# Kernel optimization log

Hardware: AMD Instinct MI355X
Metric: run time of the kernel (lower is better)

## Reference

```python
import jax, jax.numpy as jnp
import numpy as np

P, D, M, B = 32000, 128, 2, 4096
INIT_STD = 0.01


def setup_inputs() -> dict:
    key = jax.random.key(0)
    k1, k2, k3 = jax.random.split(key, 3)
    x = jax.random.randint(k1, (B, M), 0, P)                       # token indices
    W = INIT_STD * jax.random.normal(k2, (D, P), dtype=jnp.float32)
    V = INIT_STD * jax.random.normal(k3, (P, D), dtype=jnp.float32)
    return {"x": x, "W": W, "V": V}


def reference(x, W, V):
    # Original: one_hot(x, p).sum(1).T -> [p, B]; W @ x_sum == gather columns of W
    # at the token indices and sum over the m positions (identical math, no [B,p]
    # one-hot or dense GEMM materialized).
    hidden = jax.nn.relu(W[:, x].sum(axis=2))   # W[:, x]: [d, B, m] -> [d, B]
    logits = (V @ hidden).T                      # [p, B].T -> [B, p]
    return logits
```

## Files before the change

kernel.cpp:

```cpp
#include <hip/hip_runtime.h>
#include <hip/hip_bf16.h>

#define PP 32000
#define DD 128
#define BBATCH 4096

typedef __bf16 bf16x8 __attribute__((ext_vector_type(8)));
typedef float f32x4 __attribute__((ext_vector_type(4)));
typedef unsigned short ushort8 __attribute__((ext_vector_type(8)));

__device__ __forceinline__ unsigned short f2bf(float f) {
    unsigned u = __float_as_uint(f);
    u += 0x7FFFu + ((u >> 16) & 1u);
    return (unsigned short)(u >> 16);
}


__global__ void prep_hidden_kernel(const int* __restrict__ x,
                                   const float* __restrict__ W,
                                   unsigned short* __restrict__ Hb) {
    const int b = (blockIdx.x << 1) + (threadIdx.x >> 7);
    const int d = threadIdx.x & 127;
    const int i0 = x[2 * b];
    const int i1 = x[2 * b + 1];
    float h = W[(size_t)d * PP + i0] + W[(size_t)d * PP + i1];
    h = h > 0.0f ? h : 0.0f;
    const int st = ((b >> 4) << 2) | (d >> 5);
    const int l  = (((d & 31) >> 3) << 4) | (b & 15);
    Hb[(st << 9) + (l << 3) + (d & 7)] = f2bf(h);
}

__global__ void prep_v_kernel(const float* __restrict__ V,
                              unsigned short* __restrict__ Vb) {
    const int t  = blockIdx.x * 256 + threadIdx.x;
    const int l  = t & 63;
    const int st = t >> 6;
    const int ks  = st & 3;
    const int p16 = st >> 2;
    const int p  = (p16 << 4) | (l & 15);
    const int k0 = (ks << 5) | ((l >> 4) << 3);
    const float4 v0 = *reinterpret_cast<const float4*>(V + (size_t)p * DD + k0);
    const float4 v1 = *reinterpret_cast<const float4*>(V + (size_t)p * DD + k0 + 4);
    ushort8 o;
    o[0] = f2bf(v0.x); o[1] = f2bf(v0.y); o[2] = f2bf(v0.z); o[3] = f2bf(v0.w);
    o[4] = f2bf(v1.x); o[5] = f2bf(v1.y); o[6] = f2bf(v1.z); o[7] = f2bf(v1.w);
    *reinterpret_cast<ushort8*>(Vb + (size_t)t * 8) = o;
}

__global__ void gemm_kernel(const unsigned short* __restrict__ Vb,
                            const unsigned short* __restrict__ Hb,
                            float* __restrict__ out) {
    const int bid = (blockIdx.x & 7) * 1000 + (blockIdx.x >> 3);
    const int wid  = (bid << 2) + (threadIdx.x >> 6);
    const int lane = threadIdx.x & 63;
    const int bt = wid & 63;
    const int pt = wid >> 6;
    const int col = lane & 15;
    const int kq  = lane >> 4;

    const int p0 = pt << 6;
    const int b0 = bt << 6;

    const bf16x8* Abase = reinterpret_cast<const bf16x8*>(Vb) + ((pt << 4) << 6) + lane;
    const bf16x8* Bbase = reinterpret_cast<const bf16x8*>(Hb) + ((bt << 4) << 6) + lane;

    f32x4 acc[4][4];
    const f32x4 zero = {0.0f, 0.0f, 0.0f, 0.0f};
    #pragma unroll
    for (int i = 0; i < 4; ++i)
        #pragma unroll
        for (int j = 0; j < 4; ++j)
            acc[i][j] = zero;

    #pragma unroll
    for (int ks = 0; ks < 4; ++ks) {
        bf16x8 a[4], bb[4];
        #pragma unroll
        for (int i = 0; i < 4; ++i)
            a[i] = Abase[((i << 2) + ks) << 6];
        #pragma unroll
        for (int j = 0; j < 4; ++j)
            bb[j] = Bbase[((j << 2) + ks) << 6];
        #pragma unroll
        for (int i = 0; i < 4; ++i)
            #pragma unroll
            for (int j = 0; j < 4; ++j)
                acc[i][j] = __builtin_amdgcn_mfma_f32_16x16x32_bf16(
                    a[i], bb[j], acc[i][j], 0, 0, 0);
    }

    #pragma unroll
    for (int j = 0; j < 4; ++j) {
        float* row = out + (size_t)(b0 + (j << 4) + col) * PP + p0 + (kq << 2);
        #pragma unroll
        for (int i = 0; i < 4; ++i)
            __builtin_nontemporal_store(acc[i][j],
                reinterpret_cast<f32x4*>(row + (i << 4)));
    }
}

extern "C" void kernel_launch(void* const* d_in, const int* in_sizes, int n_in,
                              void* d_out, int out_size, void* d_ws, size_t ws_size,
                              hipStream_t stream) {
    const int*   x = (const int*)d_in[0];
    const float* W = (const float*)d_in[1];
    const float* V = (const float*)d_in[2];
    float* out = (float*)d_out;

    unsigned short* Hb = (unsigned short*)d_ws;
    unsigned short* Vb = Hb + (size_t)BBATCH * DD;

    prep_hidden_kernel<<<BBATCH / 2, 256, 0, stream>>>(x, W, Hb);
    prep_v_kernel<<<(PP * DD) / (8 * 256), 256, 0, stream>>>(V, Vb);
    gemm_kernel<<<8000, 256, 0, stream>>>(Vb, Hb, out);
}
```

Measured before the change: 624.3 us.

## Stage GEMM output through LDS for full-row coalesced stores

```diff
diff --git a/kernel.cpp b/kernel.cpp
--- a/kernel.cpp
+++ b/kernel.cpp
@@ -50,19 +50,22 @@
 __global__ void gemm_kernel(const unsigned short* __restrict__ Vb,
                             const unsigned short* __restrict__ Hb,
                             float* __restrict__ out) {
+    __shared__ f32x4 lds4[32 * 64];
+
     const int bid = (blockIdx.x & 7) * 1000 + (blockIdx.x >> 3);
-    const int wid  = (bid << 2) + (threadIdx.x >> 6);
+    const int PT = bid >> 6;
+    const int BT = bid & 63;
+    const int w    = threadIdx.x >> 6;
     const int lane = threadIdx.x & 63;
-    const int bt = wid & 63;
-    const int pt = wid >> 6;
     const int col = lane & 15;
     const int kq  = lane >> 4;
 
-    const int p0 = pt << 6;
-    const int b0 = bt << 6;
+    const int pt = (PT << 2) + w;
+    const int b0 = BT << 6;
+    const int P0 = PT << 8;
 
-    const bf16x8* Abase = reinterpret_cast<const bf16x8*>(Vb) + ((pt << 4) << 6) + lane;
-    const bf16x8* Bbase = reinterpret_cast<const bf16x8*>(Hb) + ((bt << 4) << 6) + lane;
+    const bf16x8* Abase = reinterpret_cast<const bf16x8*>(Vb) + (pt << 10) + lane;
+    const bf16x8* Bbase = reinterpret_cast<const bf16x8*>(Hb) + (BT << 10) + lane;
 
     f32x4 acc[4][4];
     const f32x4 zero = {0.0f, 0.0f, 0.0f, 0.0f};
@@ -90,12 +93,26 @@
     }
 
     #pragma unroll
-    for (int j = 0; j < 4; ++j) {
-        float* row = out + (size_t)(b0 + (j << 4) + col) * PP + p0 + (kq << 2);
+    for (int ph = 0; ph < 2; ++ph) {
+        if (ph) __syncthreads();
         #pragma unroll
-        for (int i = 0; i < 4; ++i)
-            __builtin_nontemporal_store(acc[i][j],
-                reinterpret_cast<f32x4*>(row + (i << 4)));
+        for (int j2 = 0; j2 < 2; ++j2) {
+            const int j = (ph << 1) + j2;
+            const int br = (j2 << 4) + col;
+            #pragma unroll
+            for (int i = 0; i < 4; ++i) {
+                const int s = (w << 4) + (i << 2) + kq;
+                lds4[(br << 6) + (s ^ br)] = acc[i][j];
+            }
+        }
+        __syncthreads();
+        #pragma unroll
+        for (int r = 0; r < 8; ++r) {
+            const int br = (w << 3) + r;
+            const f32x4 vv = lds4[(br << 6) + (lane ^ br)];
+            float* dst = out + (size_t)(b0 + (ph << 5) + br) * PP + P0 + (lane << 2);
+            __builtin_nontemporal_store(vv, reinterpret_cast<f32x4*>(dst));
+        }
     }
 }
 
```

New measurement: 557.0 us. 1.12x faster.
